# Performance work log

Measured on AMD Instinct MI355X. Metric: run time of the kernel, lower is better.

## Reference

```python
import jax, jax.numpy as jnp
import numpy as np

N_NODES = 100000
N_EDGES = 1600000
DIM_IN, DIM_H, DIM_OUT = 500, 64, 8


def setup_inputs() -> dict:
    key = jax.random.key(0)
    k_x, k_e, k_w1, k_w2 = jax.random.split(key, 4)
    x = jax.random.normal(k_x, (N_NODES, DIM_IN), dtype=jnp.float32)
    edge_index = jax.random.randint(k_e, (2, N_EDGES), 0, N_NODES, dtype=jnp.int32)
    # Glorot-ish init for linear weights, zero bias (PyG GCNConv default)
    W1 = jax.random.normal(k_w1, (DIM_IN, DIM_H), dtype=jnp.float32) * (1.0 / np.sqrt(DIM_IN))
    b1 = jnp.zeros((DIM_H,), dtype=jnp.float32)
    W2 = jax.random.normal(k_w2, (DIM_H, DIM_OUT), dtype=jnp.float32) * (1.0 / np.sqrt(DIM_H))
    b2 = jnp.zeros((DIM_OUT,), dtype=jnp.float32)
    return {"x": x, "edge_index": edge_index, "W1": W1, "b1": b1, "W2": W2, "b2": b2}


def _gcn_conv(h, W, b, src, dst, edge_norm, num_nodes):
    """GCNConv: out = D^{-1/2}(A+I)D^{-1/2} (h W) + b, via gather/scatter over edges."""
    hw = h @ W                                  # [N, d_out] dense transform
    msg = hw[src] * edge_norm[:, None]          # [E+N, d_out] gather + scale
    agg = jax.ops.segment_sum(msg, dst, num_segments=num_nodes)  # scatter-add
    return agg + b


def reference(x, edge_index, W1, b1, W2, b2):
    num_nodes = x.shape[0]
    # Add self-loops (PyG GCNConv default: add_self_loops=True)
    loops = jnp.arange(num_nodes, dtype=edge_index.dtype)
    src = jnp.concatenate([edge_index[0], loops])
    dst = jnp.concatenate([edge_index[1], loops])
    # Symmetric normalization from in-degree of loop-augmented graph
    deg = jax.ops.segment_sum(jnp.ones_like(dst, dtype=x.dtype), dst,
                              num_segments=num_nodes)
    dinv = jnp.where(deg > 0, jax.lax.rsqrt(deg), 0.0)
    edge_norm = dinv[src] * dinv[dst]           # [E+N]
    # Eval-mode forward (dropout is identity when not training)
    h = jax.nn.relu(_gcn_conv(x, W1, b1, src, dst, edge_norm, num_nodes))
    h = _gcn_conv(h, W2, b2, src, dst, edge_norm, num_nodes)
    return jax.nn.log_softmax(h, axis=1)
```

## Files before the change

### kernel.cpp

```cpp
#include <hip/hip_runtime.h>
#include <stdint.h>

#define NN 100000
#define NE 1600000
#define DIN 500
#define DH 64
#define DOUT 8
#define KP 512
#define MAXDEG 64
#define LDSW 132

#define FILL_EPT 4
#define FILL_PASSES 16
#define FILL_RS ((NN + FILL_PASSES - 1) / FILL_PASSES)

typedef __attribute__((ext_vector_type(8))) short short8;
typedef __attribute__((ext_vector_type(4))) float f32x4;
typedef unsigned short ushort_t;

static __device__ __forceinline__ ushort_t f2bf(float f) {
  union { float f; uint32_t u; } v; v.f = f;
  uint32_t u = v.u;
  return (ushort_t)((u + 0x7FFFu + ((u >> 16) & 1u)) >> 16);
}
static __device__ __forceinline__ float bf2f(ushort_t h) {
  union { uint32_t u; float f; } v; v.u = ((uint32_t)h) << 16;
  return v.f;
}

__global__ __launch_bounds__(256) void k_fill(const int* __restrict__ ei,
                                              int* __restrict__ cursor,
                                              int* __restrict__ colsrc) {
  int t = blockIdx.x * 256 + threadIdx.x;
  const int T = gridDim.x * 256;
  int s[FILL_EPT], d[FILL_EPT];
#pragma unroll
  for (int k = 0; k < FILL_EPT; ++k) {
    int id = t + k * T;
    s[k] = 0; d[k] = -1;
    if (id < NE) { s[k] = ei[id]; d[k] = ei[NE + id]; }
    else if (id < NE + NN) { s[k] = id - NE; d[k] = s[k]; }
  }
#pragma unroll 1
  for (int p = 0; p < FILL_PASSES; ++p) {
    int lo = p * FILL_RS;
    int hi = lo + FILL_RS;
#pragma unroll
    for (int k = 0; k < FILL_EPT; ++k) {
      bool act = (d[k] >= lo) && (d[k] < hi);
      if (__any(act)) {
        if (act) {
          int pos = atomicAdd(&cursor[d[k]], 1);
          if (pos < MAXDEG) colsrc[d[k] * MAXDEG + pos] = s[k];
        }
      }
    }
  }
}

__global__ __launch_bounds__(256) void k_dinv(const int* __restrict__ cursor,
                                              float* __restrict__ dinv) {
  int v = blockIdx.x * 256 + threadIdx.x;
  if (v >= NN) return;
  dinv[v] = 1.0f / sqrtf((float)cursor[v]);
}

__global__ __launch_bounds__(256) void k_w1cvt(const float* __restrict__ W1,
                                               ushort_t* __restrict__ bh,
                                               ushort_t* __restrict__ bl) {
  int id = blockIdx.x * 256 + threadIdx.x;
  if (id >= DH * KP) return;
  int i = id & 7, lane = (id >> 3) & 63, off = (id >> 9) & 3, kkg = id >> 11;
  int r = lane & 15, g = lane >> 4;
  int col = off * 16 + r;
  int k = kkg * 32 + g * 8 + i;
  float v = (k < DIN) ? W1[k * DH + col] : 0.0f;
  ushort_t hi = f2bf(v);
  bh[id] = hi;
  bl[id] = f2bf(v - bf2f(hi));
}

__global__ __launch_bounds__(256) void k_gemm1(const float* __restrict__ x,
                                               const ushort_t* __restrict__ bh,
                                               const ushort_t* __restrict__ bl,
                                               ushort_t* __restrict__ hwb) {
  __shared__ float lds[64 * LDSW];
  int tid = threadIdx.x;
  int lane = tid & 63, w = tid >> 6;
  int r = lane & 15, g = lane >> 4;
  int row0 = blockIdx.x * 64;

  f32x4 acc0 = {0,0,0,0}, acc1 = {0,0,0,0}, acc2 = {0,0,0,0}, acc3 = {0,0,0,0};

  for (int ch = 0; ch < 4; ++ch) {
    __syncthreads();
#pragma unroll
    for (int j = 0; j < 8; ++j) {
      int idx = j * 256 + tid;
      int lr = idx >> 5;
      int pos = idx & 31;
      int kq = ch * 32 + pos;
      float4 val = {0, 0, 0, 0};
      int grow = row0 + lr;
      if (kq < 125 && grow < NN)
        val = *(const float4*)(x + (size_t)grow * DIN + kq * 4);
      *(float4*)(&lds[lr * LDSW + pos * 4]) = val;
    }
    __syncthreads();
#pragma unroll
    for (int kk = 0; kk < 4; ++kk) {
      int kb = kk * 32 + g * 8;
      const float* lp = &lds[(w * 16 + r) * LDSW + kb];
      float4 v0 = *(const float4*)lp;
      float4 v1 = *(const float4*)(lp + 4);
      float a[8] = {v0.x, v0.y, v0.z, v0.w, v1.x, v1.y, v1.z, v1.w};
      short8 ah, al;
#pragma unroll
      for (int i = 0; i < 8; ++i) {
        ushort_t hi = f2bf(a[i]);
        ah[i] = (short)hi;
        al[i] = (short)f2bf(a[i] - bf2f(hi));
      }
      int kkg = ch * 4 + kk;
      const ushort_t* bph = bh + (size_t)(kkg * 4) * 512 + lane * 8;
      const ushort_t* bpl = bl + (size_t)(kkg * 4) * 512 + lane * 8;
#define TILE(T, OFF)                                                            \
      {                                                                         \
        short8 bhf = *(const short8*)(bph + (OFF) * 512);                       \
        short8 blf = *(const short8*)(bpl + (OFF) * 512);                       \
        T = __builtin_amdgcn_mfma_f32_16x16x32_bf16(ah, bhf, T, 0, 0, 0);       \
        T = __builtin_amdgcn_mfma_f32_16x16x32_bf16(al, bhf, T, 0, 0, 0);       \
        T = __builtin_amdgcn_mfma_f32_16x16x32_bf16(ah, blf, T, 0, 0, 0);       \
      }
      TILE(acc0, 0) TILE(acc1, 1) TILE(acc2, 2) TILE(acc3, 3)
#undef TILE
    }
  }
  int wrow0 = row0 + w * 16;
#pragma unroll
  for (int i = 0; i < 4; ++i) {
    int orow = wrow0 + g * 4 + i;
    if (orow < NN) {
      ushort_t* o = hwb + (size_t)orow * DH + r;
      o[0]  = f2bf(acc0[i]);
      o[16] = f2bf(acc1[i]);
      o[32] = f2bf(acc2[i]);
      o[48] = f2bf(acc3[i]);
    }
  }
}

__global__ __launch_bounds__(256) void k_agg1(const ushort_t* __restrict__ hwb,
                                              const int* __restrict__ colsrc,
                                              const int* __restrict__ cnt,
                                              const float* __restrict__ dinv,
                                              const float* __restrict__ b1,
                                              const float* __restrict__ W2,
                                              float* __restrict__ hw2) {
  int lane = threadIdx.x & 63;
  int v = blockIdx.x * 4 + (threadIdx.x >> 6);
  if (v >= NN) return;
  int c = cnt[v]; if (c > MAXDEG) c = MAXDEG;
  float dv = dinv[v];
  const int* cl = colsrc + v * MAXDEG;
  int si = cl[lane];
  bool act = lane < c;
  if (!act) si = 0;
  float nrmv = act ? dinv[si] * dv : 0.0f;
  float acc = 0.0f;
  for (int i0 = 0; i0 < c; i0 += 8) {
    float val[8];
#pragma unroll
    for (int j = 0; j < 8; ++j) {
      int s = __builtin_amdgcn_readlane(si, i0 + j);
      val[j] = bf2f(hwb[(size_t)s * DH + lane]);
    }
#pragma unroll
    for (int j = 0; j < 8; ++j) {
      float nrm = __uint_as_float(__builtin_amdgcn_readlane(__float_as_uint(nrmv), i0 + j));
      acc = fmaf(val[j], nrm, acc);
    }
  }
  float h = acc + b1[lane];
  h = h > 0.0f ? h : 0.0f;
  const float* w2r = W2 + lane * DOUT;
  float p0 = h * w2r[0], p1 = h * w2r[1], p2 = h * w2r[2], p3 = h * w2r[3];
  float p4 = h * w2r[4], p5 = h * w2r[5], p6 = h * w2r[6], p7 = h * w2r[7];
#pragma unroll
  for (int off = 32; off > 0; off >>= 1) {
    p0 += __shfl_xor(p0, off); p1 += __shfl_xor(p1, off);
    p2 += __shfl_xor(p2, off); p3 += __shfl_xor(p3, off);
    p4 += __shfl_xor(p4, off); p5 += __shfl_xor(p5, off);
    p6 += __shfl_xor(p6, off); p7 += __shfl_xor(p7, off);
  }
  if (lane == 0) {
    float4 q0 = {p0, p1, p2, p3}, q1 = {p4, p5, p6, p7};
    *(float4*)(hw2 + (size_t)v * DOUT)     = q0;
    *(float4*)(hw2 + (size_t)v * DOUT + 4) = q1;
  }
}

__global__ __launch_bounds__(256) void k_agg2(const float* __restrict__ hw2,
                                              const int* __restrict__ colsrc,
                                              const int* __restrict__ cnt,
                                              const float* __restrict__ dinv,
                                              const float* __restrict__ b2,
                                              float* __restrict__ out) {
  int lane = threadIdx.x & 63;
  int v = blockIdx.x * 4 + (threadIdx.x >> 6);
  if (v >= NN) return;
  int e = lane >> 3, f = lane & 7;
  int c = cnt[v]; if (c > MAXDEG) c = MAXDEG;
  float dv = dinv[v];
  const int* cl = colsrc + v * MAXDEG;
  float acc = 0.0f;
  for (int i0 = 0; i0 < c; i0 += 8) {
    int i = i0 + e;
    bool a2 = i < c;
    int s = a2 ? cl[i] : 0;
    float nrm = a2 ? dinv[s] * dv : 0.0f;
    float val = hw2[(size_t)s * DOUT + f] * nrm;
    val += __shfl_xor(val, 8);
    val += __shfl_xor(val, 16);
    val += __shfl_xor(val, 32);
    acc += val;
  }
  acc += b2[f];
  float m = acc;
  m = fmaxf(m, __shfl_xor(m, 1));
  m = fmaxf(m, __shfl_xor(m, 2));
  m = fmaxf(m, __shfl_xor(m, 4));
  float ex = expf(acc - m);
  float sum = ex;
  sum += __shfl_xor(sum, 1);
  sum += __shfl_xor(sum, 2);
  sum += __shfl_xor(sum, 4);
  float ls = m + logf(sum);
  if (e == 0) out[(size_t)v * DOUT + f] = acc - ls;
}

extern "C" void kernel_launch(void* const* d_in, const int* in_sizes, int n_in,
                              void* d_out, int out_size, void* d_ws, size_t ws_size,
                              hipStream_t stream) {
  const float* x  = (const float*)d_in[0];
  const int*   ei = (const int*)d_in[1];
  const float* W1 = (const float*)d_in[2];
  const float* b1 = (const float*)d_in[3];
  const float* W2 = (const float*)d_in[4];
  const float* b2 = (const float*)d_in[5];
  float* out = (float*)d_out;

  char* w = (char*)d_ws;
  size_t off = 0;
  auto alloc = [&](size_t bytes) {
    char* p = w + off;
    off += (bytes + 255) & ~(size_t)255;
    return (void*)p;
  };
  int*      cursor = (int*)alloc((size_t)NN * 4);
  float*    dinv   = (float*)alloc((size_t)NN * 4);
  ushort_t* bh     = (ushort_t*)alloc((size_t)DH * KP * 2);
  ushort_t* bl     = (ushort_t*)alloc((size_t)DH * KP * 2);
  int*      colsrc = (int*)alloc((size_t)NN * MAXDEG * 4);
  ushort_t* hwb    = (ushort_t*)alloc((size_t)NN * DH * 2);
  float*    hw2    = (float*)alloc((size_t)NN * DOUT * 4);

  hipMemsetAsync(cursor, 0, (size_t)NN * 4, stream);
  int fill_blocks = (NE + NN + 256 * FILL_EPT - 1) / (256 * FILL_EPT);
  k_fill<<<fill_blocks, 256, 0, stream>>>(ei, cursor, colsrc);
  k_dinv<<<(NN + 255) / 256, 256, 0, stream>>>(cursor, dinv);
  k_w1cvt<<<(DH * KP + 255) / 256, 256, 0, stream>>>(W1, bh, bl);
  k_gemm1<<<(NN + 63) / 64, 256, 0, stream>>>(x, bh, bl, hwb);
  k_agg1<<<(NN + 3) / 4, 256, 0, stream>>>(hwb, colsrc, cursor, dinv, b1, W2, hw2);
  k_agg2<<<(NN + 3) / 4, 256, 0, stream>>>(hw2, colsrc, cursor, dinv, b2, out);
}
```

Before: 263.0 us.

## Load GEMM1 A operands directly to registers with prefetch, interleave W1 hi/lo

The first-layer GEMM drops the LDS staging and block-wide barriers. Each wave now loads its own 16 rows of x straight into registers with nontemporal loads, prefetching the next K chunk while the MFMAs run on the current one. The W1 hi/lo bf16 split is packed into one interleaved buffer, and the B fragments are loaded up front per chunk. The layer-1 aggregation gather is also unrolled from 8 to 16 loads in flight. The cost is much higher register pressure (launch bounds set to 2 blocks) and uncoalesced per-row global loads of x.

```diff
diff --git a/kernel.cpp b/kernel.cpp
--- a/kernel.cpp
+++ b/kernel.cpp
@@ -8,7 +8,6 @@
 #define DOUT 8
 #define KP 512
 #define MAXDEG 64
-#define LDSW 132
 
 #define FILL_EPT 4
 #define FILL_PASSES 16
@@ -66,54 +65,67 @@
 }
 
 __global__ __launch_bounds__(256) void k_w1cvt(const float* __restrict__ W1,
-                                               ushort_t* __restrict__ bh,
-                                               ushort_t* __restrict__ bl) {
+                                               ushort_t* __restrict__ bt) {
   int id = blockIdx.x * 256 + threadIdx.x;
-  if (id >= DH * KP) return;
-  int i = id & 7, lane = (id >> 3) & 63, off = (id >> 9) & 3, kkg = id >> 11;
+  if (id >= DH * KP * 2) return;
+  int i = id & 7, lane = (id >> 3) & 63, h = (id >> 9) & 1;
+  int off = (id >> 10) & 3, kkg = id >> 12;
   int r = lane & 15, g = lane >> 4;
   int col = off * 16 + r;
   int k = kkg * 32 + g * 8 + i;
   float v = (k < DIN) ? W1[k * DH + col] : 0.0f;
   ushort_t hi = f2bf(v);
-  bh[id] = hi;
-  bl[id] = f2bf(v - bf2f(hi));
-}
-
-__global__ __launch_bounds__(256) void k_gemm1(const float* __restrict__ x,
-                                               const ushort_t* __restrict__ bh,
-                                               const ushort_t* __restrict__ bl,
-                                               ushort_t* __restrict__ hwb) {
-  __shared__ float lds[64 * LDSW];
-  int tid = threadIdx.x;
-  int lane = tid & 63, w = tid >> 6;
+  bt[id] = h ? f2bf(v - bf2f(hi)) : hi;
+}
+
+__global__ __launch_bounds__(256, 2) void k_gemm1(const float* __restrict__ x,
+                                                  const ushort_t* __restrict__ bt,
+                                                  ushort_t* __restrict__ hwb) {
+  int lane = threadIdx.x & 63;
+  int wid = blockIdx.x * 4 + (threadIdx.x >> 6);
+  if (wid >= NN / 16) return;
   int r = lane & 15, g = lane >> 4;
-  int row0 = blockIdx.x * 64;
+  const float* xrow = x + (size_t)(wid * 16 + r) * DIN;
 
   f32x4 acc0 = {0,0,0,0}, acc1 = {0,0,0,0}, acc2 = {0,0,0,0}, acc3 = {0,0,0,0};
-
+  f32x4 curA[8], nxtA[8];
+  const f32x4 z4 = {0, 0, 0, 0};
+
+  auto loadA = [&](f32x4* dst, int ch) {
+#pragma unroll
+    for (int kk = 0; kk < 4; ++kk) {
+      int col = ch * 128 + kk * 32 + g * 8;
+      if (ch == 3) {
+        dst[kk * 2]     = (col < DIN)     ? __builtin_nontemporal_load((const f32x4*)(xrow + col))     : z4;
+        dst[kk * 2 + 1] = (col + 4 < DIN) ? __builtin_nontemporal_load((const f32x4*)(xrow + col + 4)) : z4;
+      } else {
+        dst[kk * 2]     = __builtin_nontemporal_load((const f32x4*)(xrow + col));
+        dst[kk * 2 + 1] = __builtin_nontemporal_load((const f32x4*)(xrow + col + 4));
+      }
+    }
+  };
+
+  loadA(curA, 0);
+#pragma unroll
   for (int ch = 0; ch < 4; ++ch) {
-    __syncthreads();
-#pragma unroll
-    for (int j = 0; j < 8; ++j) {
-      int idx = j * 256 + tid;
-      int lr = idx >> 5;
-      int pos = idx & 31;
-      int kq = ch * 32 + pos;
-      float4 val = {0, 0, 0, 0};
-      int grow = row0 + lr;
-      if (kq < 125 && grow < NN)
-        val = *(const float4*)(x + (size_t)grow * DIN + kq * 4);
-      *(float4*)(&lds[lr * LDSW + pos * 4]) = val;
-    }
-    __syncthreads();
+    short8 Bh[4][4], Bl[4][4];
+#pragma unroll
+    for (int kk = 0; kk < 4; ++kk)
+#pragma unroll
+      for (int off = 0; off < 4; ++off) {
+        const ushort_t* bp = bt + (size_t)(((ch * 4 + kk) * 4 + off) * 2) * 512 + lane * 8;
+        Bh[kk][off] = *(const short8*)bp;
+        Bl[kk][off] = *(const short8*)(bp + 512);
+      }
+    __builtin_amdgcn_sched_barrier(0);
+    if (ch < 3) loadA(nxtA, ch + 1);
+    __builtin_amdgcn_sched_barrier(0);
 #pragma unroll
     for (int kk = 0; kk < 4; ++kk) {
-      int kb = kk * 32 + g * 8;
-      const float* lp = &lds[(w * 16 + r) * LDSW + kb];
-      float4 v0 = *(const float4*)lp;
-      float4 v1 = *(const float4*)(lp + 4);
-      float a[8] = {v0.x, v0.y, v0.z, v0.w, v1.x, v1.y, v1.z, v1.w};
+      float a[8];
+      f32x4 v0 = curA[kk * 2], v1 = curA[kk * 2 + 1];
+      a[0] = v0.x; a[1] = v0.y; a[2] = v0.z; a[3] = v0.w;
+      a[4] = v1.x; a[5] = v1.y; a[6] = v1.z; a[7] = v1.w;
       short8 ah, al;
 #pragma unroll
       for (int i = 0; i < 8; ++i) {
@@ -121,32 +133,25 @@
         ah[i] = (short)hi;
         al[i] = (short)f2bf(a[i] - bf2f(hi));
       }
-      int kkg = ch * 4 + kk;
-      const ushort_t* bph = bh + (size_t)(kkg * 4) * 512 + lane * 8;
-      const ushort_t* bpl = bl + (size_t)(kkg * 4) * 512 + lane * 8;
 #define TILE(T, OFF)                                                            \
-      {                                                                         \
-        short8 bhf = *(const short8*)(bph + (OFF) * 512);                       \
-        short8 blf = *(const short8*)(bpl + (OFF) * 512);                       \
-        T = __builtin_amdgcn_mfma_f32_16x16x32_bf16(ah, bhf, T, 0, 0, 0);       \
-        T = __builtin_amdgcn_mfma_f32_16x16x32_bf16(al, bhf, T, 0, 0, 0);       \
-        T = __builtin_amdgcn_mfma_f32_16x16x32_bf16(ah, blf, T, 0, 0, 0);       \
-      }
+      T = __builtin_amdgcn_mfma_f32_16x16x32_bf16(ah, Bh[kk][OFF], T, 0, 0, 0); \
+      T = __builtin_amdgcn_mfma_f32_16x16x32_bf16(al, Bh[kk][OFF], T, 0, 0, 0); \
+      T = __builtin_amdgcn_mfma_f32_16x16x32_bf16(ah, Bl[kk][OFF], T, 0, 0, 0);
       TILE(acc0, 0) TILE(acc1, 1) TILE(acc2, 2) TILE(acc3, 3)
 #undef TILE
     }
-  }
-  int wrow0 = row0 + w * 16;
+#pragma unroll
+    for (int i = 0; i < 8; ++i) curA[i] = nxtA[i];
+  }
+  int wrow0 = wid * 16;
 #pragma unroll
   for (int i = 0; i < 4; ++i) {
     int orow = wrow0 + g * 4 + i;
-    if (orow < NN) {
-      ushort_t* o = hwb + (size_t)orow * DH + r;
-      o[0]  = f2bf(acc0[i]);
-      o[16] = f2bf(acc1[i]);
-      o[32] = f2bf(acc2[i]);
-      o[48] = f2bf(acc3[i]);
-    }
+    ushort_t* o = hwb + (size_t)orow * DH + r;
+    o[0]  = f2bf(acc0[i]);
+    o[16] = f2bf(acc1[i]);
+    o[32] = f2bf(acc2[i]);
+    o[48] = f2bf(acc3[i]);
   }
 }
 
@@ -168,15 +173,15 @@
   if (!act) si = 0;
   float nrmv = act ? dinv[si] * dv : 0.0f;
   float acc = 0.0f;
-  for (int i0 = 0; i0 < c; i0 += 8) {
-    float val[8];
-#pragma unroll
-    for (int j = 0; j < 8; ++j) {
+  for (int i0 = 0; i0 < c; i0 += 16) {
+    float val[16];
+#pragma unroll
+    for (int j = 0; j < 16; ++j) {
       int s = __builtin_amdgcn_readlane(si, i0 + j);
       val[j] = bf2f(hwb[(size_t)s * DH + lane]);
     }
 #pragma unroll
-    for (int j = 0; j < 8; ++j) {
+    for (int j = 0; j < 16; ++j) {
       float nrm = __uint_as_float(__builtin_amdgcn_readlane(__float_as_uint(nrmv), i0 + j));
       acc = fmaf(val[j], nrm, acc);
     }
@@ -259,8 +264,7 @@
   };
   int*      cursor = (int*)alloc((size_t)NN * 4);
   float*    dinv   = (float*)alloc((size_t)NN * 4);
-  ushort_t* bh     = (ushort_t*)alloc((size_t)DH * KP * 2);
-  ushort_t* bl     = (ushort_t*)alloc((size_t)DH * KP * 2);
+  ushort_t* bt     = (ushort_t*)alloc((size_t)DH * KP * 2 * 2);
   int*      colsrc = (int*)alloc((size_t)NN * MAXDEG * 4);
   ushort_t* hwb    = (ushort_t*)alloc((size_t)NN * DH * 2);
   float*    hw2    = (float*)alloc((size_t)NN * DOUT * 4);
@@ -269,8 +273,8 @@
   int fill_blocks = (NE + NN + 256 * FILL_EPT - 1) / (256 * FILL_EPT);
   k_fill<<<fill_blocks, 256, 0, stream>>>(ei, cursor, colsrc);
   k_dinv<<<(NN + 255) / 256, 256, 0, stream>>>(cursor, dinv);
-  k_w1cvt<<<(DH * KP + 255) / 256, 256, 0, stream>>>(W1, bh, bl);
-  k_gemm1<<<(NN + 63) / 64, 256, 0, stream>>>(x, bh, bl, hwb);
+  k_w1cvt<<<(DH * KP * 2 + 255) / 256, 256, 0, stream>>>(W1, bt);
+  k_gemm1<<<(NN / 16 + 3) / 4, 256, 0, stream>>>(x, bt, hwb);
   k_agg1<<<(NN + 3) / 4, 256, 0, stream>>>(hwb, colsrc, cursor, dinv, b1, W2, hw2);
   k_agg2<<<(NN + 3) / 4, 256, 0, stream>>>(hw2, colsrc, cursor, dinv, b2, out);
 }
```

Measured after the change: 290.9 us. 10.6% more time.

## Double-buffer GEMM1 x tiles via register prefetch and interleave W1 hi/lo layout

Applied to the files above, without the earlier changes.

The first-layer GEMM now prefetches the next K-chunk of x into registers with nontemporal loads while the MFMAs run on the current LDS buffer. It then writes that chunk into a second LDS buffer, which removes one barrier per chunk and overlaps global loads with compute. The split-bf16 W1 hi and lo fragments are interleaved into one buffer so each tile's pair sits close together. The agg1 gather loop is also unrolled to 16 neighbors to keep more loads in flight. The cost is doubled LDS per block and more live registers, which may reduce occupancy.

```diff
diff --git a/kernel.cpp b/kernel.cpp
--- a/kernel.cpp
+++ b/kernel.cpp
@@ -66,53 +66,69 @@
 }
 
 __global__ __launch_bounds__(256) void k_w1cvt(const float* __restrict__ W1,
-                                               ushort_t* __restrict__ bh,
-                                               ushort_t* __restrict__ bl) {
+                                               ushort_t* __restrict__ bt) {
   int id = blockIdx.x * 256 + threadIdx.x;
-  if (id >= DH * KP) return;
-  int i = id & 7, lane = (id >> 3) & 63, off = (id >> 9) & 3, kkg = id >> 11;
+  if (id >= DH * KP * 2) return;
+  int i = id & 7, lane = (id >> 3) & 63, h = (id >> 9) & 1;
+  int off = (id >> 10) & 3, kkg = id >> 12;
   int r = lane & 15, g = lane >> 4;
   int col = off * 16 + r;
   int k = kkg * 32 + g * 8 + i;
   float v = (k < DIN) ? W1[k * DH + col] : 0.0f;
   ushort_t hi = f2bf(v);
-  bh[id] = hi;
-  bl[id] = f2bf(v - bf2f(hi));
+  bt[id] = h ? f2bf(v - bf2f(hi)) : hi;
 }
 
 __global__ __launch_bounds__(256) void k_gemm1(const float* __restrict__ x,
-                                               const ushort_t* __restrict__ bh,
-                                               const ushort_t* __restrict__ bl,
+                                               const ushort_t* __restrict__ bt,
                                                ushort_t* __restrict__ hwb) {
-  __shared__ float lds[64 * LDSW];
+  __shared__ float lds[2][64 * LDSW];
   int tid = threadIdx.x;
   int lane = tid & 63, w = tid >> 6;
   int r = lane & 15, g = lane >> 4;
   int row0 = blockIdx.x * 64;
 
-  f32x4 acc0 = {0,0,0,0}, acc1 = {0,0,0,0}, acc2 = {0,0,0,0}, acc3 = {0,0,0,0};
-
-  for (int ch = 0; ch < 4; ++ch) {
-    __syncthreads();
+  f32x4 st[8];
+  const f32x4 z4 = {0, 0, 0, 0};
+
+  auto loadRegs = [&](int ch) {
 #pragma unroll
     for (int j = 0; j < 8; ++j) {
       int idx = j * 256 + tid;
       int lr = idx >> 5;
-      int pos = idx & 31;
-      int kq = ch * 32 + pos;
-      float4 val = {0, 0, 0, 0};
+      int q = idx & 31;
+      int kq = ch * 32 + q;
       int grow = row0 + lr;
       if (kq < 125 && grow < NN)
-        val = *(const float4*)(x + (size_t)grow * DIN + kq * 4);
-      *(float4*)(&lds[lr * LDSW + pos * 4]) = val;
-    }
+        st[j] = __builtin_nontemporal_load((const f32x4*)(x + (size_t)grow * DIN + kq * 4));
+      else
+        st[j] = z4;
+    }
+  };
+  auto writeLDS = [&](int b) {
+#pragma unroll
+    for (int j = 0; j < 8; ++j) {
+      int idx = j * 256 + tid;
+      int lr = idx >> 5;
+      int q = idx & 31;
+      *(f32x4*)(&lds[b][lr * LDSW + q * 4]) = st[j];
+    }
+  };
+
+  f32x4 acc0 = {0,0,0,0}, acc1 = {0,0,0,0}, acc2 = {0,0,0,0}, acc3 = {0,0,0,0};
+
+  loadRegs(0);
+  writeLDS(0);
+#pragma unroll 1
+  for (int ch = 0; ch < 4; ++ch) {
     __syncthreads();
+    if (ch < 3) loadRegs(ch + 1);
+    __builtin_amdgcn_sched_barrier(0);
 #pragma unroll
     for (int kk = 0; kk < 4; ++kk) {
-      int kb = kk * 32 + g * 8;
-      const float* lp = &lds[(w * 16 + r) * LDSW + kb];
-      float4 v0 = *(const float4*)lp;
-      float4 v1 = *(const float4*)(lp + 4);
+      const float* lp = &lds[ch & 1][(w * 16 + r) * LDSW + kk * 32 + g * 8];
+      f32x4 v0 = *(const f32x4*)lp;
+      f32x4 v1 = *(const f32x4*)(lp + 4);
       float a[8] = {v0.x, v0.y, v0.z, v0.w, v1.x, v1.y, v1.z, v1.w};
       short8 ah, al;
 #pragma unroll
@@ -122,12 +138,11 @@
         al[i] = (short)f2bf(a[i] - bf2f(hi));
       }
       int kkg = ch * 4 + kk;
-      const ushort_t* bph = bh + (size_t)(kkg * 4) * 512 + lane * 8;
-      const ushort_t* bpl = bl + (size_t)(kkg * 4) * 512 + lane * 8;
+      const ushort_t* bph = bt + (size_t)(kkg * 4 * 2) * 512 + lane * 8;
 #define TILE(T, OFF)                                                            \
       {                                                                         \
-        short8 bhf = *(const short8*)(bph + (OFF) * 512);                       \
-        short8 blf = *(const short8*)(bpl + (OFF) * 512);                       \
+        short8 bhf = *(const short8*)(bph + (OFF) * 2 * 512);                   \
+        short8 blf = *(const short8*)(bph + ((OFF) * 2 + 1) * 512);             \
         T = __builtin_amdgcn_mfma_f32_16x16x32_bf16(ah, bhf, T, 0, 0, 0);       \
         T = __builtin_amdgcn_mfma_f32_16x16x32_bf16(al, bhf, T, 0, 0, 0);       \
         T = __builtin_amdgcn_mfma_f32_16x16x32_bf16(ah, blf, T, 0, 0, 0);       \
@@ -135,6 +150,8 @@
       TILE(acc0, 0) TILE(acc1, 1) TILE(acc2, 2) TILE(acc3, 3)
 #undef TILE
     }
+    __builtin_amdgcn_sched_barrier(0);
+    if (ch < 3) writeLDS((ch + 1) & 1);
   }
   int wrow0 = row0 + w * 16;
 #pragma unroll
@@ -168,15 +185,15 @@
   if (!act) si = 0;
   float nrmv = act ? dinv[si] * dv : 0.0f;
   float acc = 0.0f;
-  for (int i0 = 0; i0 < c; i0 += 8) {
-    float val[8];
-#pragma unroll
-    for (int j = 0; j < 8; ++j) {
+  for (int i0 = 0; i0 < c; i0 += 16) {
+    float val[16];
+#pragma unroll
+    for (int j = 0; j < 16; ++j) {
       int s = __builtin_amdgcn_readlane(si, i0 + j);
       val[j] = bf2f(hwb[(size_t)s * DH + lane]);
     }
 #pragma unroll
-    for (int j = 0; j < 8; ++j) {
+    for (int j = 0; j < 16; ++j) {
       float nrm = __uint_as_float(__builtin_amdgcn_readlane(__float_as_uint(nrmv), i0 + j));
       acc = fmaf(val[j], nrm, acc);
     }
@@ -259,8 +276,7 @@
   };
   int*      cursor = (int*)alloc((size_t)NN * 4);
   float*    dinv   = (float*)alloc((size_t)NN * 4);
-  ushort_t* bh     = (ushort_t*)alloc((size_t)DH * KP * 2);
-  ushort_t* bl     = (ushort_t*)alloc((size_t)DH * KP * 2);
+  ushort_t* bt     = (ushort_t*)alloc((size_t)DH * KP * 2 * 2);
   int*      colsrc = (int*)alloc((size_t)NN * MAXDEG * 4);
   ushort_t* hwb    = (ushort_t*)alloc((size_t)NN * DH * 2);
   float*    hw2    = (float*)alloc((size_t)NN * DOUT * 4);
@@ -269,8 +285,8 @@
   int fill_blocks = (NE + NN + 256 * FILL_EPT - 1) / (256 * FILL_EPT);
   k_fill<<<fill_blocks, 256, 0, stream>>>(ei, cursor, colsrc);
   k_dinv<<<(NN + 255) / 256, 256, 0, stream>>>(cursor, dinv);
-  k_w1cvt<<<(DH * KP + 255) / 256, 256, 0, stream>>>(W1, bh, bl);
-  k_gemm1<<<(NN + 63) / 64, 256, 0, stream>>>(x, bh, bl, hwb);
+  k_w1cvt<<<(DH * KP * 2 + 255) / 256, 256, 0, stream>>>(W1, bt);
+  k_gemm1<<<(NN + 63) / 64, 256, 0, stream>>>(x, bt, hwb);
   k_agg1<<<(NN + 3) / 4, 256, 0, stream>>>(hwb, colsrc, cursor, dinv, b1, W2, hw2);
   k_agg2<<<(NN + 3) / 4, 256, 0, stream>>>(hw2, colsrc, cursor, dinv, b2, out);
 }
```

After: 279.4 us. 6.2% more time.
